# Kernel optimization log

Measured on AMD Instinct MI355X. Metric: run time of the kernel, lower is better.

The kernel has to match this reference:

```python
import jax, jax.numpy as jnp
import numpy as np

D_MODEL = 1024
N_HEADS = 16
D_K = D_MODEL // N_HEADS
D_FF = 4 * D_MODEL
MEM = 32
EPS = 1e-6
NEG = -1e9


def layer_norm(x, alpha, bias):
    # torch: alpha * (x - mean) / (std_unbiased + eps) + bias
    mean = jnp.mean(x, axis=-1, keepdims=True)
    std = jnp.sqrt(jnp.var(x, axis=-1, keepdims=True, ddof=1))
    return alpha * (x - mean) / (std + EPS) + bias


def setup_inputs() -> dict:
    key = jax.random.key(0)
    ks = jax.random.split(key, 12)
    B, S = 4, 2048
    s = 1.0 / np.sqrt(D_MODEL)
    inp = {
        "x": jax.random.normal(ks[0], (B, S, D_MODEL), jnp.float32),
        "mask": jnp.ones((1, 1, S, S + MEM), jnp.int32),
        "memory_tokens": jax.random.normal(ks[1], (MEM, D_MODEL), jnp.float32),
        "w_q": jax.random.normal(ks[2], (D_MODEL, D_MODEL), jnp.float32) * s,
        "w_k": jax.random.normal(ks[3], (D_MODEL, D_MODEL), jnp.float32) * s,
        "w_v": jax.random.normal(ks[4], (D_MODEL, D_MODEL), jnp.float32) * s,
        "w_o": jax.random.normal(ks[5], (D_MODEL, D_MODEL), jnp.float32) * s,
        "ln1_alpha": jnp.ones((D_MODEL,), jnp.float32),
        "ln1_bias": jnp.zeros((D_MODEL,), jnp.float32),
        "ln2_alpha": jnp.ones((D_MODEL,), jnp.float32),
        "ln2_bias": jnp.zeros((D_MODEL,), jnp.float32),
        "ff_w1": jax.random.normal(ks[6], (D_MODEL, D_FF), jnp.float32) * s,
        "ff_b1": jnp.zeros((D_FF,), jnp.float32),
        "ff_w2": jax.random.normal(ks[7], (D_FF, D_MODEL), jnp.float32) * (1.0 / np.sqrt(D_FF)),
        "ff_b2": jnp.zeros((D_MODEL,), jnp.float32),
    }
    return inp


def reference(x, mask, memory_tokens, w_q, w_k, w_v, w_o,
              ln1_alpha, ln1_bias, ln2_alpha, ln2_bias,
              ff_w1, ff_b1, ff_w2, ff_b2):
    B, S, D = x.shape
    memory = jnp.broadcast_to(memory_tokens[None], (B, MEM, D))

    # --- residual 1: self attention with memory K/V ---
    xn = layer_norm(x, ln1_alpha, ln1_bias)
    q = (xn @ w_q).reshape(B, S, N_HEADS, D_K).transpose(0, 2, 1, 3)  # [B,h,S,dk]
    k = (xn @ w_k).reshape(B, S, N_HEADS, D_K).transpose(0, 2, 1, 3)
    v = (xn @ w_v).reshape(B, S, N_HEADS, D_K).transpose(0, 2, 1, 3)
    mem_k = (memory @ w_k).reshape(B, MEM, N_HEADS, D_K).transpose(0, 2, 1, 3)
    mem_v = (memory @ w_v).reshape(B, MEM, N_HEADS, D_K).transpose(0, 2, 1, 3)
    k = jnp.concatenate([mem_k, k], axis=2)  # [B,h,M+S,dk]
    v = jnp.concatenate([mem_v, v], axis=2)

    scores = jnp.einsum("bhsd,bhtd->bhst", q, k) / np.sqrt(D_K)  # [B,h,S,M+S]
    scores = jnp.where(mask == 0, NEG, scores)
    attn = jax.nn.softmax(scores, axis=-1)
    ctx = jnp.einsum("bhst,bhtd->bhsd", attn, v)
    ctx = ctx.transpose(0, 2, 1, 3).reshape(B, S, D)
    x = x + ctx @ w_o

    # --- residual 2: FFN ---
    xn2 = layer_norm(x, ln2_alpha, ln2_bias)
    ff = jax.nn.relu(xn2 @ ff_w1 + ff_b1) @ ff_w2 + ff_b2
    x = x + ff

    new_memory = jnp.broadcast_to(jnp.mean(x, axis=1, keepdims=True), (B, MEM, D))
    return (x, new_memory)
```

## Files before the change

kernel.cpp:

```cpp
#include <hip/hip_runtime.h>
#include <hip/hip_bf16.h>
#include <cstdint>
#include <cstddef>


typedef __attribute__((ext_vector_type(8))) short short8;
typedef __attribute__((ext_vector_type(4))) float floatx4;
typedef __attribute__((ext_vector_type(4))) unsigned short ushort4v;

#define NB   4
#define SEQ  2048
#define DM   1024
#define DKH  64
#define TT   2080
#define DFF  4096
#define NMEM 32

static __device__ __forceinline__ float bu2f(unsigned short u) {
  return __uint_as_float(((unsigned int)u) << 16);
}
static __device__ __forceinline__ unsigned short f2bu(float x) {
  __hip_bfloat16 h = __float2bfloat16(x);
  return *reinterpret_cast<unsigned short*>(&h);
}
static __device__ __forceinline__ float fast_exp2(float x) {
#if __has_builtin(__builtin_amdgcn_exp2f)
  return __builtin_amdgcn_exp2f(x);
#else
  return exp2f(x);
#endif
}
static __device__ __forceinline__ void async16(const void* g, void* l) {
  __builtin_amdgcn_global_load_lds(
      (const __attribute__((address_space(1))) void*)g,
      (__attribute__((address_space(3))) void*)l, 16, 0, 0);
}

#define PREP_X   8192
#define PREP_MT  (PREP_X + 32)
#define PREP_SM  (PREP_MT + 9)
#define PREP_T   (PREP_SM + 3072)

__global__ __launch_bounds__(256) void prep(
    const void* __restrict__ x,   const void* __restrict__ memtok,
    const void* __restrict__ wq,  const void* __restrict__ wk,
    const void* __restrict__ wv,  const void* __restrict__ wo,
    const void* __restrict__ fw1, const void* __restrict__ fw2,
    const void* __restrict__ ln1a, const void* __restrict__ ln1b,
    const void* __restrict__ ln2a, const void* __restrict__ ln2b,
    const void* __restrict__ fb1, const void* __restrict__ fb2,
    unsigned short* __restrict__ xb, unsigned short* __restrict__ MT,
    unsigned short* __restrict__ Wtq, unsigned short* __restrict__ Wtk,
    unsigned short* __restrict__ Wtv, unsigned short* __restrict__ Wto,
    unsigned short* __restrict__ Wt1, unsigned short* __restrict__ Wt2,
    unsigned short* __restrict__ L1A, unsigned short* __restrict__ L1B,
    unsigned short* __restrict__ L2A, unsigned short* __restrict__ L2B,
    unsigned short* __restrict__ FB1, unsigned short* __restrict__ FB2,
    int* __restrict__ FLAG)
{
  const int tid = threadIdx.x;
  const unsigned short probe = ((const unsigned short*)x)[tid & 63];
  const unsigned e = (probe >> 7) & 0xFF;
  const bool ok = (e == 0) || (e >= 100 && e <= 141);
  const int flag = (__ballot(!ok) != 0ULL) ? 1 : 0;
  const int bid = blockIdx.x;
  if (bid == 0 && tid == 0) *FLAG = flag;

  if (bid < PREP_T && bid >= PREP_SM) {
    const int tb = bid - PREP_SM;
    const void* in; unsigned short* outp; int R, C, tx, ty;
    if (tb < 1024) {
      const int w = tb >> 8, lt = tb & 255;
      in = (w == 0) ? wq : (w == 1) ? wk : (w == 2) ? wv : wo;
      outp = (w == 0) ? Wtq : (w == 1) ? Wtk : (w == 2) ? Wtv : Wto;
      R = DM; C = DM; tx = lt & 15; ty = lt >> 4;
    } else if (tb < 2048) {
      const int lt = tb - 1024;
      in = fw1; outp = Wt1; R = DM; C = DFF; tx = lt & 63; ty = lt >> 6;
    } else {
      const int lt = tb - 2048;
      in = fw2; outp = Wt2; R = DFF; C = DM; tx = lt & 15; ty = lt >> 4;
    }
    __shared__ unsigned short tile[64][65];
    const int r0 = ty << 6, c0 = tx << 6;
    const int lr = tid >> 2, lc = (tid & 3) << 4;
    if (flag) {
      const float* ip = (const float*)in + (size_t)(r0 + lr) * C + c0 + lc;
#pragma unroll
      for (int q = 0; q < 16; q += 4) {
        floatx4 f = *(const floatx4*)(ip + q);
        tile[lr][lc+q+0] = f2bu(f[0]); tile[lr][lc+q+1] = f2bu(f[1]);
        tile[lr][lc+q+2] = f2bu(f[2]); tile[lr][lc+q+3] = f2bu(f[3]);
      }
    } else {
      const unsigned short* ip = (const unsigned short*)in + (size_t)(r0 + lr) * C + c0 + lc;
#pragma unroll
      for (int q = 0; q < 16; q += 4) {
        ushort4v a = *(const ushort4v*)(ip + q);
        tile[lr][lc+q+0] = a.x; tile[lr][lc+q+1] = a.y;
        tile[lr][lc+q+2] = a.z; tile[lr][lc+q+3] = a.w;
      }
    }
    __syncthreads();
    unsigned short* op = outp + (size_t)(c0 + lr) * R + r0 + lc;
#pragma unroll
    for (int q = 0; q < 16; q += 4) {
      ushort4v a;
      a.x = tile[lc+q+0][lr]; a.y = tile[lc+q+1][lr];
      a.z = tile[lc+q+2][lr]; a.w = tile[lc+q+3][lr];
      *(ushort4v*)(op + q) = a;
    }
    return;
  }

  const void* src; unsigned short* dst; int base;
  if (bid < PREP_X)      { src = x;      dst = xb; base = bid * 1024; }
  else if (bid < PREP_MT){ src = memtok; dst = MT; base = (bid - PREP_X) * 1024; }
  else {
    const int s = bid - PREP_MT; base = 0;
    if      (s == 0) { src = ln1a; dst = L1A; }
    else if (s == 1) { src = ln1b; dst = L1B; }
    else if (s == 2) { src = ln2a; dst = L2A; }
    else if (s == 3) { src = ln2b; dst = L2B; }
    else if (s <= 7) { src = fb1;  dst = FB1; base = (s - 4) * 1024; }
    else             { src = fb2;  dst = FB2; }
  }
  const int i = base + tid * 4;
  if (flag) {
    const float* s4 = (const float*)src + i;
    ushort4v o;
    o.x = f2bu(s4[0]); o.y = f2bu(s4[1]); o.z = f2bu(s4[2]); o.w = f2bu(s4[3]);
    *(ushort4v*)&dst[i] = o;
  } else {
    *(ushort4v*)&dst[i] = *(const ushort4v*)&((const unsigned short*)src)[i];
  }
}

__global__ __launch_bounds__(256, 2) void gemm_bt(
    const unsigned short* __restrict__ A, int lda,
    const unsigned short* __restrict__ Bt, int ldbt,
    const unsigned short* __restrict__ bias,
    const unsigned short* __restrict__ resid_b,
    const float* __restrict__ resid_f,
    void* __restrict__ outp,
    int M, int N, int K, int relu, int mode, const int* __restrict__ dt)
{
  __shared__ __align__(16) unsigned short As[128 * 32];
  __shared__ __align__(16) unsigned short Bs[128 * 32];

  const int tid  = threadIdx.x;
  const int wave = tid >> 6;
  const int lane = tid & 63;
  const int quad = lane >> 4;
  const int lr   = lane & 15;
  const int wm   = (wave >> 1) * 64;
  const int wn   = (wave & 1) * 64;
  const int m0   = blockIdx.y * 128;
  const int n0   = blockIdx.x * 128;

  floatx4 acc[4][4];
#pragma unroll
  for (int i = 0; i < 4; ++i)
#pragma unroll
    for (int j = 0; j < 4; ++j) { floatx4 z = {0.f, 0.f, 0.f, 0.f}; acc[i][j] = z; }

  const int srow = lane >> 2;
  const int skof = (((lane & 3) ^ ((lane >> 3) & 3))) * 8;
  const int fsw  = (lr >> 1) & 3;

  for (int k0 = 0; k0 < K; k0 += 32) {
#pragma unroll
    for (int i = 0; i < 2; ++i) {
      const int r = wave * 32 + i * 16 + srow;
      int gr = m0 + r; gr = gr < M ? gr : (M - 1);
      async16(A  + (size_t)gr * lda + k0 + skof, &As[(wave * 32 + i * 16) * 32]);
      const int gn = n0 + r;
      async16(Bt + (size_t)gn * ldbt + k0 + skof, &Bs[(wave * 32 + i * 16) * 32]);
    }
    __syncthreads();
    short8 af[4], bfr[4];
#pragma unroll
    for (int mi = 0; mi < 4; ++mi)
      af[mi]  = *(const short8*)&As[(wm + mi * 16 + lr) * 32 + ((quad ^ fsw) * 8)];
#pragma unroll
    for (int ni = 0; ni < 4; ++ni)
      bfr[ni] = *(const short8*)&Bs[(wn + ni * 16 + lr) * 32 + ((quad ^ fsw) * 8)];
#pragma unroll
    for (int mi = 0; mi < 4; ++mi)
#pragma unroll
      for (int ni = 0; ni < 4; ++ni)
        acc[mi][ni] = __builtin_amdgcn_mfma_f32_16x16x32_bf16(af[mi], bfr[ni], acc[mi][ni], 0, 0, 0);
    __syncthreads();
  }

  if (mode == 2) {
#pragma unroll
    for (int mi = 0; mi < 4; ++mi) {
      const int rb = m0 + wm + mi * 16 + quad * 4;
#pragma unroll
      for (int ni = 0; ni < 4; ++ni) {
        const int col = n0 + wn + ni * 16 + lr;
        int bb, t;
        if (rb < NB * SEQ) { bb = rb >> 11; t = NMEM + (rb & (SEQ - 1)); }
        else               { bb = 0;        t = rb - NB * SEQ; }
        unsigned short* op = (unsigned short*)outp + ((size_t)bb * DM + col) * TT + t;
        if (rb + 3 < M) {
          ushort4v pk;
          pk.x = f2bu(acc[mi][ni][0]); pk.y = f2bu(acc[mi][ni][1]);
          pk.z = f2bu(acc[mi][ni][2]); pk.w = f2bu(acc[mi][ni][3]);
          *(ushort4v*)op = pk;
        } else {
#pragma unroll
          for (int rg = 0; rg < 4; ++rg)
            if (rb + rg < M) op[rg] = f2bu(acc[mi][ni][rg]);
        }
      }
    }
    return;
  }

  const int ofp32 = (mode == 4 && dt) ? *dt : 0;
#pragma unroll
  for (int mi = 0; mi < 4; ++mi) {
    const int rb = m0 + wm + mi * 16 + quad * 4;
#pragma unroll
    for (int ni = 0; ni < 4; ++ni) {
      const int col = n0 + wn + ni * 16 + lr;
      const float bv = bias ? bu2f(bias[col]) : 0.0f;
#pragma unroll
      for (int rg = 0; rg < 4; ++rg) {
        const int r = rb + rg;
        if (r >= M) continue;
        float v = acc[mi][ni][rg] + bv;
        if (relu) v = fmaxf(v, 0.0f);
        if (resid_b) v += bu2f(resid_b[(size_t)r * N + col]);
        if (resid_f) v += resid_f[(size_t)r * N + col];
        size_t idx;
        if (mode == 1) {
          const int row2 = (r < NB * SEQ) ? ((r >> 11) * TT + NMEM + (r & (SEQ - 1)))
                                          : (r - NB * SEQ);
          idx = (size_t)row2 * DM + col;
        } else {
          idx = (size_t)r * N + col;
        }
        if (mode == 3)       ((float*)outp)[idx] = v;
        else if (mode == 4) {
          if (ofp32) ((float*)outp)[idx] = v;
          else       ((unsigned short*)outp)[idx] = f2bu(v);
        } else               ((unsigned short*)outp)[idx] = f2bu(v);
      }
    }
  }
}

#define PSTR 72

__global__ __launch_bounds__(256, 4) void flash_attn(
    const unsigned short* __restrict__ Q,
    const unsigned short* __restrict__ Kb,
    const unsigned short* __restrict__ Vtb,
    unsigned short* __restrict__ ctx)
{
  __shared__ __align__(16) unsigned short Ks[64 * 64];
  __shared__ __align__(16) unsigned short Vs[64 * 64];
  __shared__ __align__(16) unsigned short Ps[128 * PSTR];

  const int tid  = threadIdx.x;
  const int wave = tid >> 6;
  const int lane = tid & 63;
  const int quad = lane >> 4;
  const int lr   = lane & 15;

  const int i    = blockIdx.x;
  const int pair = (i & 7) * 8 + (i >> 7);
  const int q0   = ((i >> 3) & 15) * 128;
  const int b    = pair >> 4;
  const int h    = pair & 15;

  const unsigned short* Qb  = Q   + ((size_t)(b * SEQ + q0)) * DM + h * DKH;
  const unsigned short* Kbp = Kb  + ((size_t)b * TT) * DM + h * DKH;
  const unsigned short* Vbp = Vtb + ((size_t)(b * DM + h * DKH)) * TT;

  short8 aq[2][2];
#pragma unroll
  for (int mi = 0; mi < 2; ++mi)
#pragma unroll
    for (int ks = 0; ks < 2; ++ks)
      aq[mi][ks] = *(const short8*)(Qb + (size_t)(wave * 32 + mi * 16 + lr) * DM
                                       + ks * 32 + quad * 8);

  const int srl = lane >> 3;
  const int swc = (lane & 7) ^ srl;

  floatx4 O[2][4], Osum[2];
#pragma unroll
  for (int mi = 0; mi < 2; ++mi) {
    floatx4 z = {0.f, 0.f, 0.f, 0.f};
    Osum[mi] = z;
#pragma unroll
    for (int ni = 0; ni < 4; ++ni) O[mi][ni] = z;
  }
  short8 ones;
#pragma unroll
  for (int i2 = 0; i2 < 8; ++i2) ones[i2] = (short)0x3F80;

  const float SC = 0.125f * 1.4426950408889634f;

  for (int t0 = 0; t0 < TT; t0 += 64) {
    __syncthreads();
#pragma unroll
    for (int i2 = 0; i2 < 2; ++i2) {
      const int rr = (wave * 2 + i2) * 8 + srl;
      int tg = t0 + rr; tg = tg < TT ? tg : (TT - 1);
      async16(Kbp + (size_t)tg * DM + swc * 8, &Ks[(wave * 2 + i2) * 512]);
      int ts = t0 + swc * 8; ts = ts <= (TT - 8) ? ts : (TT - 8);
      async16(Vbp + (size_t)rr * TT + ts, &Vs[(wave * 2 + i2) * 512]);
    }
    __syncthreads();

    floatx4 sc4[2][4];
#pragma unroll
    for (int mi = 0; mi < 2; ++mi)
#pragma unroll
      for (int ni = 0; ni < 4; ++ni) { floatx4 z = {0.f, 0.f, 0.f, 0.f}; sc4[mi][ni] = z; }
#pragma unroll
    for (int ks = 0; ks < 2; ++ks) {
      short8 bk[4];
#pragma unroll
      for (int ni = 0; ni < 4; ++ni) {
        const int row = ni * 16 + lr;
        bk[ni] = *(const short8*)&Ks[row * 64 + (((ks * 4 + quad) ^ (row & 7)) * 8)];
      }
#pragma unroll
      for (int mi = 0; mi < 2; ++mi)
#pragma unroll
        for (int ni = 0; ni < 4; ++ni)
          sc4[mi][ni] = __builtin_amdgcn_mfma_f32_16x16x32_bf16(aq[mi][ks], bk[ni], sc4[mi][ni], 0, 0, 0);
    }

    bool valid[4];
#pragma unroll
    for (int ni = 0; ni < 4; ++ni) valid[ni] = (t0 + ni * 16 + lr) < TT;

#pragma unroll
    for (int mi = 0; mi < 2; ++mi)
#pragma unroll
      for (int rg = 0; rg < 4; ++rg) {
        const int prow = wave * 32 + mi * 16 + quad * 4 + rg;
#pragma unroll
        for (int ni = 0; ni < 4; ++ni) {
          const float p = valid[ni] ? fast_exp2(sc4[mi][ni][rg] * SC) : 0.0f;
          Ps[prow * PSTR + ni * 16 + lr] =
              (unsigned short)((__float_as_uint(p) + 0x8000u) >> 16);
        }
      }

    __asm__ __volatile__("" ::: "memory");

#pragma unroll
    for (int ks = 0; ks < 2; ++ks) {
      short8 ap[2], bv[4];
#pragma unroll
      for (int mi = 0; mi < 2; ++mi)
        ap[mi] = *(const short8*)&Ps[(wave * 32 + mi * 16 + lr) * PSTR + ks * 32 + quad * 8];
#pragma unroll
      for (int ni = 0; ni < 4; ++ni) {
        const int row = ni * 16 + lr;
        bv[ni] = *(const short8*)&Vs[row * 64 + (((ks * 4 + quad) ^ (row & 7)) * 8)];
      }
#pragma unroll
      for (int mi = 0; mi < 2; ++mi) {
        Osum[mi] = __builtin_amdgcn_mfma_f32_16x16x32_bf16(ap[mi], ones, Osum[mi], 0, 0, 0);
#pragma unroll
        for (int ni = 0; ni < 4; ++ni)
          O[mi][ni] = __builtin_amdgcn_mfma_f32_16x16x32_bf16(ap[mi], bv[ni], O[mi][ni], 0, 0, 0);
      }
    }
  }

#pragma unroll
  for (int mi = 0; mi < 2; ++mi)
#pragma unroll
    for (int rg = 0; rg < 4; ++rg) {
      const float inv = 1.0f / Osum[mi][rg];
      const int row = q0 + wave * 32 + mi * 16 + quad * 4 + rg;
#pragma unroll
      for (int ni = 0; ni < 4; ++ni) {
        const int col = h * DKH + ni * 16 + lr;
        ctx[((size_t)(b * SEQ + row)) * DM + col] = f2bu(O[mi][ni][rg] * inv);
      }
    }
}

__global__ __launch_bounds__(256) void ln_kernel(
    const unsigned short* __restrict__ xin_bf,
    const float* __restrict__ xin_f,
    const unsigned short* __restrict__ memtok,
    const unsigned short* __restrict__ gam,
    const unsigned short* __restrict__ bet,
    unsigned short* __restrict__ outp,
    int rows_main)
{
  const int row = blockIdx.x;
  const int tid = threadIdx.x;
  const int c0  = tid * 4;
  if (row >= rows_main) {
    const int mr = row - rows_main;
    *(ushort4v*)&outp[(size_t)row * DM + c0] =
        *(const ushort4v*)&memtok[(size_t)mr * DM + c0];
    return;
  }
  float v[4];
  if (xin_bf) {
    ushort4v u = *(const ushort4v*)&xin_bf[(size_t)row * DM + c0];
    v[0] = bu2f(u.x); v[1] = bu2f(u.y); v[2] = bu2f(u.z); v[3] = bu2f(u.w);
  } else {
    floatx4 f = *(const floatx4*)&xin_f[(size_t)row * DM + c0];
    v[0] = f[0]; v[1] = f[1]; v[2] = f[2]; v[3] = f[3];
  }
  float s  = v[0] + v[1] + v[2] + v[3];
  float ss = v[0]*v[0] + v[1]*v[1] + v[2]*v[2] + v[3]*v[3];
#pragma unroll
  for (int m = 1; m <= 32; m <<= 1) {
    s  += __shfl_xor(s, m, 64);
    ss += __shfl_xor(ss, m, 64);
  }
  __shared__ float red[8];
  const int wave = tid >> 6, lane = tid & 63;
  if (lane == 0) { red[wave] = s; red[4 + wave] = ss; }
  __syncthreads();
  s  = red[0] + red[1] + red[2] + red[3];
  ss = red[4] + red[5] + red[6] + red[7];
  const float mean = s * (1.0f / 1024.0f);
  float var = (ss - 1024.0f * mean * mean) * (1.0f / 1023.0f);
  var = fmaxf(var, 0.0f);
  const float inv = 1.0f / (sqrtf(var) + 1e-6f);
  ushort4v o;
  o.x = f2bu(bu2f(gam[c0+0]) * (v[0] - mean) * inv + bu2f(bet[c0+0]));
  o.y = f2bu(bu2f(gam[c0+1]) * (v[1] - mean) * inv + bu2f(bet[c0+1]));
  o.z = f2bu(bu2f(gam[c0+2]) * (v[2] - mean) * inv + bu2f(bet[c0+2]));
  o.w = f2bu(bu2f(gam[c0+3]) * (v[3] - mean) * inv + bu2f(bet[c0+3]));
  *(ushort4v*)&outp[(size_t)row * DM + c0] = o;
}

__global__ __launch_bounds__(256) void replicate_mem(
    unsigned short* __restrict__ Kb, unsigned short* __restrict__ Vtb)
{
  const int idx = blockIdx.x * 256 + threadIdx.x;
  const int t = idx >> 10, c = idx & 1023;
  const unsigned short kv = Kb[(size_t)t * DM + c];
  const unsigned short vv = Vtb[(size_t)c * TT + t];
#pragma unroll
  for (int b = 1; b < NB; ++b) {
    Kb[((size_t)b * TT + t) * DM + c] = kv;
    Vtb[((size_t)(b * DM + c)) * TT + t] = vv;
  }
}

__global__ __launch_bounds__(256) void colsum(
    const void* __restrict__ xo, float* __restrict__ acc,
    const int* __restrict__ flag)
{
  const int d  = blockIdx.x * 256 + threadIdx.x;
  const int s0 = blockIdx.y * 256;
  const int b  = blockIdx.z;
  const size_t base = ((size_t)(b * SEQ + s0)) * DM + d;
  float s = 0.0f;
  if (*flag) {
    const float* p = (const float*)xo;
    for (int i = 0; i < 256; ++i) s += p[base + (size_t)i * DM];
  } else {
    const unsigned short* p = (const unsigned short*)xo;
    for (int i = 0; i < 256; ++i) s += bu2f(p[base + (size_t)i * DM]);
  }
  atomicAdd(&acc[b * DM + d], s);
}

__global__ __launch_bounds__(256) void write_mem(
    const float* __restrict__ acc, void* __restrict__ dout,
    const int* __restrict__ flag)
{
  const int idx = blockIdx.x * 256 + threadIdx.x;
  const int b = idx >> 10, d = idx & 1023;
  const float w = acc[idx] * (1.0f / 2048.0f);
  const int f = *flag;
#pragma unroll
  for (int m = 0; m < NMEM; ++m) {
    const size_t off = (size_t)NB * SEQ * DM + ((size_t)(b * NMEM + m)) * DM + d;
    if (f) ((float*)dout)[off] = w;
    else   ((unsigned short*)dout)[off] = f2bu(w);
  }
}

extern "C" void kernel_launch(void* const* d_in, const int* in_sizes, int n_in,
                              void* d_out, int out_size, void* d_ws, size_t ws_size,
                              hipStream_t stream) {
  const void* x      = d_in[0];
  const void* memtok = d_in[2];
  const void* wq     = d_in[3];
  const void* wk     = d_in[4];
  const void* wv     = d_in[5];
  const void* wo     = d_in[6];
  const void* ln1a   = d_in[7];
  const void* ln1b   = d_in[8];
  const void* ln2a   = d_in[9];
  const void* ln2b   = d_in[10];
  const void* fw1    = d_in[11];
  const void* fb1    = d_in[12];
  const void* fw2    = d_in[13];
  const void* fb2    = d_in[14];

  char* ws = (char*)d_ws;
  constexpr size_t OFF_WT1 = 0;
  constexpr size_t OFF_WT2 = OFF_WT1 + (size_t)DFF * DM * 2;
  constexpr size_t OFF_VT  = OFF_WT2 + (size_t)DM * DFF * 2;
  constexpr size_t SZ_VT   = (size_t)NB * DM * TT * 2;
  constexpr size_t OFF_Q   = OFF_VT + SZ_VT;
  constexpr size_t SZ_Q    = (size_t)NB * SEQ * DM * 2;
  constexpr size_t OFF_K   = OFF_Q + SZ_Q;
  constexpr size_t SZ_K    = (size_t)NB * TT * DM * 2;
  constexpr size_t OFF_XN  = OFF_K + SZ_K;
  constexpr size_t SZ_XN   = (size_t)8224 * DM * 2;
  constexpr size_t OFF_W4  = OFF_XN + SZ_XN;
  constexpr size_t SZ_DD   = (size_t)DM * DM * 2;
  constexpr size_t OFF_XB  = OFF_W4 + 4 * SZ_DD;
  constexpr size_t SZ_XB   = (size_t)NB * SEQ * DM * 2;
  constexpr size_t OFF_SM  = OFF_XB + SZ_XB;
  static_assert(OFF_XN + (size_t)NB * SEQ * 2048 * 2 <= OFF_SM, "h1 overlay");
  static_assert(OFF_Q + (size_t)NB * SEQ * DM * 4 <= OFF_XN, "x1f overlay");

  unsigned short* Wt1 = (unsigned short*)(ws + OFF_WT1);
  unsigned short* Wt2 = (unsigned short*)(ws + OFF_WT2);
  unsigned short* Vtb = (unsigned short*)(ws + OFF_VT);
  unsigned short* Qb  = (unsigned short*)(ws + OFF_Q);
  unsigned short* Kbf = (unsigned short*)(ws + OFF_K);
  unsigned short* xn  = (unsigned short*)(ws + OFF_XN);
  unsigned short* Wtq = (unsigned short*)(ws + OFF_W4);
  unsigned short* Wtk = (unsigned short*)(ws + OFF_W4 + SZ_DD);
  unsigned short* Wtv = (unsigned short*)(ws + OFF_W4 + 2 * SZ_DD);
  unsigned short* Wto = (unsigned short*)(ws + OFF_W4 + 3 * SZ_DD);
  unsigned short* xb  = (unsigned short*)(ws + OFF_XB);
  unsigned short* MT  = (unsigned short*)(ws + OFF_SM);
  unsigned short* L1A = (unsigned short*)(ws + OFF_SM + 65536);
  unsigned short* L1B = (unsigned short*)(ws + OFF_SM + 67584);
  unsigned short* L2A = (unsigned short*)(ws + OFF_SM + 69632);
  unsigned short* L2B = (unsigned short*)(ws + OFF_SM + 71680);
  unsigned short* FB1 = (unsigned short*)(ws + OFF_SM + 73728);
  unsigned short* FB2 = (unsigned short*)(ws + OFF_SM + 81920);
  float*          accb= (float*)(ws + OFF_SM + 84480);
  int*            FLAG= (int*)(ws + OFF_SM + 101376);

  unsigned short* ctx = xn;
  unsigned short* h1  = xn;
  float*          x1f = (float*)(ws + OFF_Q);
  unsigned short* xn2 = Vtb;

  const dim3 blk(256);

  prep<<<PREP_T, blk, 0, stream>>>(x, memtok, wq, wk, wv, wo, fw1, fw2,
                                   ln1a, ln1b, ln2a, ln2b, fb1, fb2,
                                   xb, MT, Wtq, Wtk, Wtv, Wto, Wt1, Wt2,
                                   L1A, L1B, L2A, L2B, FB1, FB2, FLAG);

  ln_kernel<<<8224, blk, 0, stream>>>(xb, nullptr, MT, L1A, L1B, xn, 8192);

  gemm_bt<<<dim3(8, 64), blk, 0, stream>>>(xn, DM, Wtq, DM, nullptr, nullptr, nullptr, Qb,  8192, DM, DM, 0, 0, nullptr);
  gemm_bt<<<dim3(8, 65), blk, 0, stream>>>(xn, DM, Wtk, DM, nullptr, nullptr, nullptr, Kbf, 8224, DM, DM, 0, 1, nullptr);
  gemm_bt<<<dim3(8, 65), blk, 0, stream>>>(xn, DM, Wtv, DM, nullptr, nullptr, nullptr, Vtb, 8224, DM, DM, 0, 2, nullptr);
  replicate_mem<<<128, blk, 0, stream>>>(Kbf, Vtb);

  flash_attn<<<1024, blk, 0, stream>>>(Qb, Kbf, Vtb, ctx);

  gemm_bt<<<dim3(8, 64), blk, 0, stream>>>(ctx, DM, Wto, DM, nullptr, xb, nullptr, x1f, 8192, DM, DM, 0, 3, nullptr);

  ln_kernel<<<8192, blk, 0, stream>>>(nullptr, x1f, nullptr, L2A, L2B, xn2, 8192);

  gemm_bt<<<dim3(16, 64), blk, 0, stream>>>(xn2, DM, Wt1, DM, FB1, nullptr, nullptr, h1, 8192, 2048, DM, 1, 0, nullptr);
  gemm_bt<<<dim3(8, 64),  blk, 0, stream>>>(h1, 2048, Wt2, DFF, nullptr, nullptr, x1f, x1f, 8192, DM, 2048, 0, 3, nullptr);
  gemm_bt<<<dim3(16, 64), blk, 0, stream>>>(xn2, DM, Wt1 + (size_t)2048 * DM, DM, FB1 + 2048, nullptr, nullptr, h1, 8192, 2048, DM, 1, 0, nullptr);
  gemm_bt<<<dim3(8, 64),  blk, 0, stream>>>(h1, 2048, Wt2 + 2048, DFF, FB2, nullptr, x1f, d_out, 8192, DM, 2048, 0, 4, FLAG);

  hipMemsetAsync(accb, 0, (size_t)NB * DM * sizeof(float), stream);
  colsum<<<dim3(4, 8, 4), blk, 0, stream>>>(d_out, accb, FLAG);
  write_mem<<<16, blk, 0, stream>>>(accb, d_out, FLAG);
}
```

Baseline: 715.5 us.

## Double-buffer GEMM LDS tiles and remap workgroups across XCDs

Splits the GEMM shared-memory tiles into two buffers so the async global-to-LDS loads for the next K step are issued before computing the current one, using explicit vmcnt waits and raw barriers. Also remaps the linear workgroup index so consecutive tiles land on the same XCD, aiming for better L2 reuse. This doubles LDS use, which may reduce occupancy, and the swizzle assumes the workgroup count is divisible by 8.

Measured after the change: 688.0 us. 3.8% less time.

```diff
diff --git a/kernel.cpp b/kernel.cpp
--- a/kernel.cpp
+++ b/kernel.cpp
@@ -145,8 +145,8 @@
     void* __restrict__ outp,
     int M, int N, int K, int relu, int mode, const int* __restrict__ dt)
 {
-  __shared__ __align__(16) unsigned short As[128 * 32];
-  __shared__ __align__(16) unsigned short Bs[128 * 32];
+  __shared__ __align__(16) unsigned short As[2][128 * 32];
+  __shared__ __align__(16) unsigned short Bs[2][128 * 32];
 
   const int tid  = threadIdx.x;
   const int wave = tid >> 6;
@@ -155,8 +155,15 @@
   const int lr   = lane & 15;
   const int wm   = (wave >> 1) * 64;
   const int wn   = (wave & 1) * 64;
-  const int m0   = blockIdx.y * 128;
-  const int n0   = blockIdx.x * 128;
+
+  const int gx  = gridDim.x;
+  const int nwg = gx * gridDim.y;
+  int wg = blockIdx.y * gx + blockIdx.x;
+  wg = (wg & 7) * (nwg >> 3) + (wg >> 3);
+  const int by = wg / gx;
+  const int bx = wg - by * gx;
+  const int m0 = by * 128;
+  const int n0 = bx * 128;
 
   floatx4 acc[4][4];
 #pragma unroll
@@ -168,29 +175,48 @@
   const int skof = (((lane & 3) ^ ((lane >> 3) & 3))) * 8;
   const int fsw  = (lr >> 1) & 3;
 
-  for (int k0 = 0; k0 < K; k0 += 32) {
+  auto stage = [&](int buf, int kk) {
 #pragma unroll
     for (int i = 0; i < 2; ++i) {
-      const int r = wave * 32 + i * 16 + srow;
+      const int rr = wave * 32 + i * 16;
+      const int r  = rr + srow;
       int gr = m0 + r; gr = gr < M ? gr : (M - 1);
-      async16(A  + (size_t)gr * lda + k0 + skof, &As[(wave * 32 + i * 16) * 32]);
+      async16(A  + (size_t)gr * lda + kk + skof, &As[buf][rr * 32]);
       const int gn = n0 + r;
-      async16(Bt + (size_t)gn * ldbt + k0 + skof, &Bs[(wave * 32 + i * 16) * 32]);
-    }
-    __syncthreads();
+      async16(Bt + (size_t)gn * ldbt + kk + skof, &Bs[buf][rr * 32]);
+    }
+  };
+
+  const int nk = K >> 5;
+  stage(0, 0);
+  int cur = 0;
+  for (int it = 0; it < nk; ++it) {
+    if (it + 1 < nk) {
+      stage(cur ^ 1, (it + 1) << 5);
+      asm volatile("s_waitcnt vmcnt(4)" ::: "memory");
+    } else {
+      asm volatile("s_waitcnt vmcnt(0)" ::: "memory");
+    }
+    __builtin_amdgcn_s_barrier();
+
+    const unsigned short* Ab = &As[cur][0];
+    const unsigned short* Bb = &Bs[cur][0];
     short8 af[4], bfr[4];
 #pragma unroll
     for (int mi = 0; mi < 4; ++mi)
-      af[mi]  = *(const short8*)&As[(wm + mi * 16 + lr) * 32 + ((quad ^ fsw) * 8)];
+      af[mi]  = *(const short8*)&Ab[(wm + mi * 16 + lr) * 32 + ((quad ^ fsw) * 8)];
 #pragma unroll
     for (int ni = 0; ni < 4; ++ni)
-      bfr[ni] = *(const short8*)&Bs[(wn + ni * 16 + lr) * 32 + ((quad ^ fsw) * 8)];
+      bfr[ni] = *(const short8*)&Bb[(wn + ni * 16 + lr) * 32 + ((quad ^ fsw) * 8)];
 #pragma unroll
     for (int mi = 0; mi < 4; ++mi)
 #pragma unroll
       for (int ni = 0; ni < 4; ++ni)
         acc[mi][ni] = __builtin_amdgcn_mfma_f32_16x16x32_bf16(af[mi], bfr[ni], acc[mi][ni], 0, 0, 0);
-    __syncthreads();
+
+    asm volatile("s_waitcnt lgkmcnt(0)" ::: "memory");
+    __builtin_amdgcn_s_barrier();
+    cur ^= 1;
   }
 
   if (mode == 2) {
```
